# Performance work log

Hardware: AMD Instinct MI355X
Metric: run time of the kernel (lower is better)

## Reference

```python
import jax, jax.numpy as jnp
import numpy as np

N_NODES = 50000


def _gcn_conv(x, src, dst, W, b, n):
    # PyG GCNConv: linear transform, add self-loops, symmetric norm, scatter-sum, bias.
    h = x @ W  # [N, out]
    loop = jnp.arange(n, dtype=src.dtype)
    s = jnp.concatenate([src, loop])
    d = jnp.concatenate([dst, loop])
    deg = jax.ops.segment_sum(jnp.ones_like(d, dtype=h.dtype), d, num_segments=n)
    dinv = jax.lax.rsqrt(jnp.maximum(deg, 1.0))  # deg >= 1 thanks to self-loops
    norm = dinv[s] * dinv[d]  # [E+N]
    msg = h[s] * norm[:, None]
    out = jax.ops.segment_sum(msg, d, num_segments=n)
    return out + b


def setup_inputs() -> dict:
    key = jax.random.key(0)
    ks = jax.random.split(key, 8)
    N, E = N_NODES, 800000
    d_in, d_hid, d_out = 128, 64, 128
    x = jax.random.normal(ks[0], (N, d_in), dtype=jnp.float32)
    edge_index = jax.random.randint(ks[1], (2, E), 0, N, dtype=jnp.int64)
    s = 1.0 / np.sqrt(d_in)
    W1 = jax.random.normal(ks[2], (d_in, d_hid), dtype=jnp.float32) * s
    b1 = jnp.zeros((d_hid,), dtype=jnp.float32)
    Wl = jax.random.normal(ks[3], (d_hid, d_out), dtype=jnp.float32) * (1.0 / np.sqrt(d_hid))
    bl = jnp.zeros((d_out,), dtype=jnp.float32)
    W2 = jax.random.normal(ks[4], (d_hid, d_out), dtype=jnp.float32) * (1.0 / np.sqrt(d_hid))
    b2 = jnp.zeros((d_out,), dtype=jnp.float32)
    return {"x": x, "edge_index": edge_index, "W1": W1, "b1": b1,
            "Wl": Wl, "bl": bl, "W2": W2, "b2": b2}


def reference(x, edge_index, W1, b1, Wl, bl, W2, b2):
    n = x.shape[0]
    src, dst = edge_index[0], edge_index[1]
    h = _gcn_conv(x, src, dst, W1, b1, n)          # conv1 -> [N, 64]
    x1 = h @ Wl + bl                               # residual linear branch [N, 128]
    h = jax.nn.relu(h)
    out = _gcn_conv(h, src, dst, W2, b2, n)        # conv2 -> [N, 128]
    return out + x + x1
```

## Files before the change

kernel.cpp:

```cpp
#include <hip/hip_runtime.h>
#include <hip/hip_fp16.h>

#define DIN 128
#define DH 64
#define DOUT 128
#define STRIDE 64
#define NPART 4


typedef _Float16 f16x8 __attribute__((ext_vector_type(8)));
typedef float f32x4 __attribute__((ext_vector_type(4)));

__global__ __launch_bounds__(256) void k_fill(const int* __restrict__ src,
                                              const int* __restrict__ dst,
                                              int* __restrict__ cnt,
                                              unsigned short* __restrict__ csr,
                                              int E, int n) {
  const int part = blockIdx.x & (NPART - 1);
  const int pb = blockIdx.x >> 2;
  const int nblk = gridDim.x >> 2;
  const int lo = (int)((long)part * n / NPART);
  const int hi = (int)((long)(part + 1) * n / NPART);
  for (int e = pb * 256 + threadIdx.x; e < E; e += nblk * 256) {
    int d = dst[e];
    if (d >= lo && d < hi) {
      int slot = atomicAdd(&cnt[d], 1);
      if (slot < STRIDE) csr[(long)d * STRIDE + slot] = (unsigned short)src[e];
    }
  }
}

__global__ __launch_bounds__(256) void k_gemm1m(const float* __restrict__ x,
                                                const float* __restrict__ W1,
                                                const int* __restrict__ cnt,
                                                __half* __restrict__ h0p, int n) {
  __shared__ _Float16 As[32][DIN + 8];
  __shared__ _Float16 Bt[DH][DIN + 8];
  __shared__ float dds[32];
  const int t = threadIdx.x;
  const int row0 = blockIdx.x * 32;
  if (t < 32) {
    int row = row0 + t;
    dds[t] = (row < n) ? rsqrtf(1.0f + (float)min(cnt[row], STRIDE)) : 0.f;
  }
  for (int i = t; i < DIN * DH; i += 256) {
    int k = i >> 6, c = i & 63;
    Bt[c][k] = (_Float16)W1[i];
  }
  for (int i = t; i < 32 * (DIN / 4); i += 256) {
    int r = i >> 5, k4 = (i & 31) * 4;
    float4 v = make_float4(0.f, 0.f, 0.f, 0.f);
    int row = row0 + r;
    if (row < n) v = *(const float4*)&x[(long)row * DIN + k4];
    As[r][k4 + 0] = (_Float16)v.x; As[r][k4 + 1] = (_Float16)v.y;
    As[r][k4 + 2] = (_Float16)v.z; As[r][k4 + 3] = (_Float16)v.w;
  }
  __syncthreads();

  const int w = t >> 6, l = t & 63;
  const int rg = w & 1;
  const int cg0 = (w >> 1) * 2;
  const int ia = l & 15, kg = l >> 4;
  f32x4 acc0 = {0.f, 0.f, 0.f, 0.f}, acc1 = {0.f, 0.f, 0.f, 0.f};
#pragma unroll
  for (int kb = 0; kb < DIN; kb += 32) {
    f16x8 a  = *(const f16x8*)&As[rg * 16 + ia][kb + kg * 8];
    f16x8 b0 = *(const f16x8*)&Bt[cg0 * 16 + ia][kb + kg * 8];
    f16x8 b1 = *(const f16x8*)&Bt[(cg0 + 1) * 16 + ia][kb + kg * 8];
    acc0 = __builtin_amdgcn_mfma_f32_16x16x32_f16(a, b0, acc0, 0, 0, 0);
    acc1 = __builtin_amdgcn_mfma_f32_16x16x32_f16(a, b1, acc1, 0, 0, 0);
  }
#pragma unroll
  for (int reg = 0; reg < 4; reg++) {
    int rr = rg * 16 + kg * 4 + reg;
    int row = row0 + rr;
    if (row < n) {
      float dd = dds[rr];
      h0p[(long)row * DH + cg0 * 16 + ia] = (__half)(acc0[reg] * dd);
      h0p[(long)row * DH + (cg0 + 1) * 16 + ia] = (__half)(acc1[reg] * dd);
    }
  }
}

__global__ __launch_bounds__(256) void k_gather1(const int* __restrict__ cnt,
                                                 const unsigned short* __restrict__ csr,
                                                 const __half* __restrict__ h0p,
                                                 const float* __restrict__ b1,
                                                 __half* __restrict__ hd, int n) {
  long gid = (long)blockIdx.x * 256 + threadIdx.x;
  int node = (int)(gid >> 3);
  if (node >= n) return;
  int l = (int)(gid & 7);
  const int deg = min(cnt[node], STRIDE);
  const float dd = rsqrtf(1.0f + (float)deg);
  const long base = (long)node * STRIDE;
  float acc[8];
#pragma unroll
  for (int k = 0; k < 8; k++) acc[k] = 0.f;

  auto edge = [&](int s) {
    union { uint4 u; __half2 h[4]; } c;
    c.u = *(const uint4*)&h0p[(long)s * DH + l * 8];
#pragma unroll
    for (int k = 0; k < 4; k++) {
      float2 f = __half22float2(c.h[k]);
      acc[2 * k] += f.x;
      acc[2 * k + 1] += f.y;
    }
  };

  int j = 0;
  for (; j + 4 <= deg; j += 4) {
    ushort4 cs = *(const ushort4*)&csr[base + j];
    edge(cs.x); edge(cs.y); edge(cs.z); edge(cs.w);
  }
  for (; j < deg; j++) edge(csr[base + j]);
  edge(node);

  float4 ba = *(const float4*)&b1[l * 8];
  float4 bb = *(const float4*)&b1[l * 8 + 4];
  float o[8];
  o[0] = acc[0] * dd + ba.x; o[1] = acc[1] * dd + ba.y;
  o[2] = acc[2] * dd + ba.z; o[3] = acc[3] * dd + ba.w;
  o[4] = acc[4] * dd + bb.x; o[5] = acc[5] * dd + bb.y;
  o[6] = acc[6] * dd + bb.z; o[7] = acc[7] * dd + bb.w;
  union { uint4 u; __half2 h[4]; } rv;
#pragma unroll
  for (int k = 0; k < 4; k++)
    rv.h[k] = __floats2half2_rn(o[2 * k] * dd, o[2 * k + 1] * dd);
  *(uint4*)&hd[(long)node * DH + l * 8] = rv.u;
}

__global__ __launch_bounds__(256) void k_gather2C(const int* __restrict__ cnt,
                                                  const unsigned short* __restrict__ csr,
                                                  const __half* __restrict__ hd,
                                                  const float* __restrict__ Wl,
                                                  const float* __restrict__ W2,
                                                  const float* __restrict__ bl,
                                                  const float* __restrict__ b2,
                                                  const float* __restrict__ x,
                                                  float* __restrict__ out, int n) {
  __shared__ float hs[32][DH + 4];
  const int t = threadIdx.x;
  const int row0 = blockIdx.x * 32;

  {
    const int r = t >> 3;
    const int l = t & 7;
    int node = row0 + r;
    float acc[8];
#pragma unroll
    for (int k = 0; k < 8; k++) acc[k] = 0.f;
    float dd = 0.f;
    if (node < n) {
      const int deg = min(cnt[node], STRIDE);
      dd = rsqrtf(1.0f + (float)deg);
      const long base = (long)node * STRIDE;
      auto edge = [&](int s) {
        union { uint4 u; __half2 h[4]; } c;
        c.u = *(const uint4*)&hd[(long)s * DH + l * 8];
#pragma unroll
        for (int k = 0; k < 4; k++) {
          float2 f = __half22float2(c.h[k]);
          acc[2 * k] += fmaxf(f.x, 0.f);
          acc[2 * k + 1] += fmaxf(f.y, 0.f);
        }
      };
      int j = 0;
      for (; j + 4 <= deg; j += 4) {
        ushort4 cs = *(const ushort4*)&csr[base + j];
        edge(cs.x); edge(cs.y); edge(cs.z); edge(cs.w);
      }
      for (; j < deg; j++) edge(csr[base + j]);
      edge(node);
    }
    *(float4*)&hs[r][l * 8] =
        make_float4(acc[0] * dd, acc[1] * dd, acc[2] * dd, acc[3] * dd);
    *(float4*)&hs[r][l * 8 + 4] =
        make_float4(acc[4] * dd, acc[5] * dd, acc[6] * dd, acc[7] * dd);
  }

  const int tc = t & 31, tr = t >> 5;
  const int col4 = tc * 4, r0 = tr * 4;
  float acc[4][4];
#pragma unroll
  for (int r = 0; r < 4; r++)
#pragma unroll
    for (int c = 0; c < 4; c++) acc[r][c] = 0.f;

  __syncthreads();
  for (int k4 = 0; k4 < DH; k4 += 4) {
    float4 hv[4];
#pragma unroll
    for (int r = 0; r < 4; r++) hv[r] = *(const float4*)&hs[r0 + r][k4];
#pragma unroll
    for (int kk = 0; kk < 4; kk++) {
      float4 wv = *(const float4*)&W2[(k4 + kk) * DOUT + col4];
#pragma unroll
      for (int r = 0; r < 4; r++) {
        float hval = (&hv[r].x)[kk];
        acc[r][0] = fmaf(hval, wv.x, acc[r][0]);
        acc[r][1] = fmaf(hval, wv.y, acc[r][1]);
        acc[r][2] = fmaf(hval, wv.z, acc[r][2]);
        acc[r][3] = fmaf(hval, wv.w, acc[r][3]);
      }
    }
  }
  __syncthreads();

  {
    const int r = t >> 3;
    const int l8 = (t & 7) * 8;
    int row = row0 + r;
    float v[8];
#pragma unroll
    for (int k = 0; k < 8; k++) v[k] = 0.f;
    if (row < n) {
      float sc = sqrtf(1.0f + (float)min(cnt[row], STRIDE));
      union { uint4 u; __half2 h[4]; } c;
      c.u = *(const uint4*)&hd[(long)row * DH + l8];
#pragma unroll
      for (int k = 0; k < 4; k++) {
        float2 f = __half22float2(c.h[k]);
        v[2 * k] = f.x * sc;
        v[2 * k + 1] = f.y * sc;
      }
    }
    *(float4*)&hs[r][l8] = make_float4(v[0], v[1], v[2], v[3]);
    *(float4*)&hs[r][l8 + 4] = make_float4(v[4], v[5], v[6], v[7]);
  }
  __syncthreads();
  for (int k4 = 0; k4 < DH; k4 += 4) {
    float4 hv[4];
#pragma unroll
    for (int r = 0; r < 4; r++) hv[r] = *(const float4*)&hs[r0 + r][k4];
#pragma unroll
    for (int kk = 0; kk < 4; kk++) {
      float4 wv = *(const float4*)&Wl[(k4 + kk) * DOUT + col4];
#pragma unroll
      for (int r = 0; r < 4; r++) {
        float hval = (&hv[r].x)[kk];
        acc[r][0] = fmaf(hval, wv.x, acc[r][0]);
        acc[r][1] = fmaf(hval, wv.y, acc[r][1]);
        acc[r][2] = fmaf(hval, wv.z, acc[r][2]);
        acc[r][3] = fmaf(hval, wv.w, acc[r][3]);
      }
    }
  }

  float4 blv = *(const float4*)&bl[col4];
  float4 b2v = *(const float4*)&b2[col4];
#pragma unroll
  for (int r = 0; r < 4; r++) {
    int row = row0 + r0 + r;
    if (row < n) {
      float4 xv = *(const float4*)&x[(long)row * DOUT + col4];
      float4 o;
      o.x = xv.x + acc[r][0] + blv.x + b2v.x;
      o.y = xv.y + acc[r][1] + blv.y + b2v.y;
      o.z = xv.z + acc[r][2] + blv.z + b2v.z;
      o.w = xv.w + acc[r][3] + blv.w + b2v.w;
      *(float4*)&out[(long)row * DOUT + col4] = o;
    }
  }
}

extern "C" void kernel_launch(void* const* d_in, const int* in_sizes, int n_in,
                              void* d_out, int out_size, void* d_ws, size_t ws_size,
                              hipStream_t stream) {
  const float* x = (const float*)d_in[0];
  const int* edge_index = (const int*)d_in[1];
  const float* W1 = (const float*)d_in[2];
  const float* b1 = (const float*)d_in[3];
  const float* Wl = (const float*)d_in[4];
  const float* bl = (const float*)d_in[5];
  const float* W2 = (const float*)d_in[6];
  const float* b2 = (const float*)d_in[7];
  float* out = (float*)d_out;

  const int n = in_sizes[0] / DIN;
  const int E = in_sizes[1] / 2;
  const int* src = edge_index;
  const int* dst = edge_index + E;

  char* p = (char*)d_ws;
  auto alloc = [&](size_t bytes) { char* r = p; p += (bytes + 255) & ~(size_t)255; return r; };
  int* cnt = (int*)alloc((size_t)n * 4);
  unsigned short* csr = (unsigned short*)alloc((size_t)n * STRIDE * 2);
  __half* h0p = (__half*)alloc((size_t)n * DH * 2);
  __half* hd = (__half*)alloc((size_t)n * DH * 2);

  const int B = 256;
  const int blocks32 = (n + 31) / 32;
  hipMemsetAsync(cnt, 0, (size_t)n * sizeof(int), stream);
  k_fill<<<NPART * 256, B, 0, stream>>>(src, dst, cnt, csr, E, n);
  k_gemm1m<<<blocks32, B, 0, stream>>>(x, W1, cnt, h0p, n);
  k_gather1<<<(int)(((long)n * 8 + B - 1) / B), B, 0, stream>>>(cnt, csr, h0p, b1, hd, n);
  k_gather2C<<<blocks32, B, 0, stream>>>(cnt, csr, hd, Wl, W2, bl, b2, x, out, n);
}
```

Measured before the change: 197.0 us.

## Use MFMA f16 matrix cores for fused conv2 and residual GEMMs

Replaces the scalar FP32 FMA loops in the final fused kernel with MFMA 16x16x32 f16 instructions. W2 and Wl are pre-transposed to fp16 by a new small kernel and staged through shared memory. The aggregated features and the rescaled residual input are converted to fp16 as MFMA operands. This removes most of the VALU work in the epilogue GEMMs, at the cost of an extra launch, extra syncs, fp16 rounding of intermediates, and output stores that are no longer vectorised.

After: 188.9 us (median of 2 runs). 1.04x faster.

```diff
diff --git a/kernel.cpp b/kernel.cpp
--- a/kernel.cpp
+++ b/kernel.cpp
@@ -30,6 +30,18 @@
   }
 }
 
+__global__ __launch_bounds__(256) void k_wt(const float* __restrict__ W2,
+                                            const float* __restrict__ Wl,
+                                            __half* __restrict__ Wt2g,
+                                            __half* __restrict__ Wtlg) {
+  int i = blockIdx.x * 256 + threadIdx.x;
+  if (i < DH * DOUT) {
+    int k = i >> 7, c = i & 127;
+    Wt2g[c * DH + k] = __float2half(W2[i]);
+    Wtlg[c * DH + k] = __float2half(Wl[i]);
+  }
+}
+
 __global__ __launch_bounds__(256) void k_gemm1m(const float* __restrict__ x,
                                                 const float* __restrict__ W1,
                                                 const int* __restrict__ cnt,
@@ -131,18 +143,25 @@
   *(uint4*)&hd[(long)node * DH + l * 8] = rv.u;
 }
 
-__global__ __launch_bounds__(256) void k_gather2C(const int* __restrict__ cnt,
+__global__ __launch_bounds__(256) void k_gather2M(const int* __restrict__ cnt,
                                                   const unsigned short* __restrict__ csr,
                                                   const __half* __restrict__ hd,
-                                                  const float* __restrict__ Wl,
-                                                  const float* __restrict__ W2,
+                                                  const __half* __restrict__ Wt2g,
+                                                  const __half* __restrict__ Wtlg,
                                                   const float* __restrict__ bl,
                                                   const float* __restrict__ b2,
                                                   const float* __restrict__ x,
                                                   float* __restrict__ out, int n) {
-  __shared__ float hs[32][DH + 4];
+  __shared__ _Float16 Wt[DOUT][DH + 8];
+  __shared__ _Float16 zs[32][DH + 8];
+  __shared__ float scs[32];
   const int t = threadIdx.x;
   const int row0 = blockIdx.x * 32;
+
+  for (int i = t; i < DOUT * (DH / 8); i += 256) {
+    int c = i >> 3, kq = (i & 7) * 8;
+    *(f16x8*)&Wt[c][kq] = *(const f16x8*)&Wt2g[c * DH + kq];
+  }
 
   {
     const int r = t >> 3;
@@ -174,93 +193,64 @@
       for (; j < deg; j++) edge(csr[base + j]);
       edge(node);
     }
-    *(float4*)&hs[r][l * 8] =
-        make_float4(acc[0] * dd, acc[1] * dd, acc[2] * dd, acc[3] * dd);
-    *(float4*)&hs[r][l * 8 + 4] =
-        make_float4(acc[4] * dd, acc[5] * dd, acc[6] * dd, acc[7] * dd);
-  }
-
-  const int tc = t & 31, tr = t >> 5;
-  const int col4 = tc * 4, r0 = tr * 4;
-  float acc[4][4];
-#pragma unroll
-  for (int r = 0; r < 4; r++)
-#pragma unroll
-    for (int c = 0; c < 4; c++) acc[r][c] = 0.f;
-
-  __syncthreads();
-  for (int k4 = 0; k4 < DH; k4 += 4) {
-    float4 hv[4];
-#pragma unroll
-    for (int r = 0; r < 4; r++) hv[r] = *(const float4*)&hs[r0 + r][k4];
-#pragma unroll
-    for (int kk = 0; kk < 4; kk++) {
-      float4 wv = *(const float4*)&W2[(k4 + kk) * DOUT + col4];
-#pragma unroll
-      for (int r = 0; r < 4; r++) {
-        float hval = (&hv[r].x)[kk];
-        acc[r][0] = fmaf(hval, wv.x, acc[r][0]);
-        acc[r][1] = fmaf(hval, wv.y, acc[r][1]);
-        acc[r][2] = fmaf(hval, wv.z, acc[r][2]);
-        acc[r][3] = fmaf(hval, wv.w, acc[r][3]);
+    if (l == 0)
+      scs[r] = (node < n) ? sqrtf(1.0f + (float)min(cnt[node], STRIDE)) : 0.f;
+    f16x8 zv;
+#pragma unroll
+    for (int k = 0; k < 8; k++) zv[k] = (_Float16)(acc[k] * dd);
+    *(f16x8*)&zs[r][l * 8] = zv;
+  }
+  __syncthreads();
+
+  const int w = t >> 6, l = t & 63;
+  const int rg = w & 1;
+  const int cb = (w >> 1) * 4;
+  const int ia = l & 15, kg = l >> 4;
+  f32x4 acc[4];
+#pragma unroll
+  for (int c = 0; c < 4; c++) acc[c] = (f32x4){0.f, 0.f, 0.f, 0.f};
+
+#pragma unroll
+  for (int kb = 0; kb < DH; kb += 32) {
+    f16x8 a = *(const f16x8*)&zs[rg * 16 + ia][kb + kg * 8];
+#pragma unroll
+    for (int c = 0; c < 4; c++) {
+      f16x8 b = *(const f16x8*)&Wt[(cb + c) * 16 + ia][kb + kg * 8];
+      acc[c] = __builtin_amdgcn_mfma_f32_16x16x32_f16(a, b, acc[c], 0, 0, 0);
+    }
+  }
+  __syncthreads();
+  for (int i = t; i < DOUT * (DH / 8); i += 256) {
+    int c = i >> 3, kq = (i & 7) * 8;
+    *(f16x8*)&Wt[c][kq] = *(const f16x8*)&Wtlg[c * DH + kq];
+  }
+  __syncthreads();
+
+  {
+    int rr = min(row0 + rg * 16 + ia, n - 1);
+    _Float16 sc = (_Float16)scs[rg * 16 + ia];
+    const _Float16* hrow = (const _Float16*)&hd[(long)rr * DH];
+#pragma unroll
+    for (int kb = 0; kb < DH; kb += 32) {
+      f16x8 a = *(const f16x8*)&hrow[kb + kg * 8];
+      a *= sc;
+#pragma unroll
+      for (int c = 0; c < 4; c++) {
+        f16x8 b = *(const f16x8*)&Wt[(cb + c) * 16 + ia][kb + kg * 8];
+        acc[c] = __builtin_amdgcn_mfma_f32_16x16x32_f16(a, b, acc[c], 0, 0, 0);
       }
     }
   }
-  __syncthreads();
-
-  {
-    const int r = t >> 3;
-    const int l8 = (t & 7) * 8;
-    int row = row0 + r;
-    float v[8];
-#pragma unroll
-    for (int k = 0; k < 8; k++) v[k] = 0.f;
-    if (row < n) {
-      float sc = sqrtf(1.0f + (float)min(cnt[row], STRIDE));
-      union { uint4 u; __half2 h[4]; } c;
-      c.u = *(const uint4*)&hd[(long)row * DH + l8];
-#pragma unroll
-      for (int k = 0; k < 4; k++) {
-        float2 f = __half22float2(c.h[k]);
-        v[2 * k] = f.x * sc;
-        v[2 * k + 1] = f.y * sc;
-      }
-    }
-    *(float4*)&hs[r][l8] = make_float4(v[0], v[1], v[2], v[3]);
-    *(float4*)&hs[r][l8 + 4] = make_float4(v[4], v[5], v[6], v[7]);
-  }
-  __syncthreads();
-  for (int k4 = 0; k4 < DH; k4 += 4) {
-    float4 hv[4];
-#pragma unroll
-    for (int r = 0; r < 4; r++) hv[r] = *(const float4*)&hs[r0 + r][k4];
-#pragma unroll
-    for (int kk = 0; kk < 4; kk++) {
-      float4 wv = *(const float4*)&Wl[(k4 + kk) * DOUT + col4];
-#pragma unroll
-      for (int r = 0; r < 4; r++) {
-        float hval = (&hv[r].x)[kk];
-        acc[r][0] = fmaf(hval, wv.x, acc[r][0]);
-        acc[r][1] = fmaf(hval, wv.y, acc[r][1]);
-        acc[r][2] = fmaf(hval, wv.z, acc[r][2]);
-        acc[r][3] = fmaf(hval, wv.w, acc[r][3]);
-      }
-    }
-  }
-
-  float4 blv = *(const float4*)&bl[col4];
-  float4 b2v = *(const float4*)&b2[col4];
-#pragma unroll
-  for (int r = 0; r < 4; r++) {
-    int row = row0 + r0 + r;
-    if (row < n) {
-      float4 xv = *(const float4*)&x[(long)row * DOUT + col4];
-      float4 o;
-      o.x = xv.x + acc[r][0] + blv.x + b2v.x;
-      o.y = xv.y + acc[r][1] + blv.y + b2v.y;
-      o.z = xv.z + acc[r][2] + blv.z + b2v.z;
-      o.w = xv.w + acc[r][3] + blv.w + b2v.w;
-      *(float4*)&out[(long)row * DOUT + col4] = o;
+
+#pragma unroll
+  for (int c = 0; c < 4; c++) {
+    const int col = (cb + c) * 16 + ia;
+    const float bc = bl[col] + b2[col];
+#pragma unroll
+    for (int reg = 0; reg < 4; reg++) {
+      int row = row0 + rg * 16 + kg * 4 + reg;
+      if (row < n)
+        out[(long)row * DOUT + col] = acc[c][reg] + x[(long)row * DOUT + col] + bc;
     }
   }
 }
@@ -289,12 +279,15 @@
   unsigned short* csr = (unsigned short*)alloc((size_t)n * STRIDE * 2);
   __half* h0p = (__half*)alloc((size_t)n * DH * 2);
   __half* hd = (__half*)alloc((size_t)n * DH * 2);
+  __half* Wt2g = (__half*)alloc((size_t)DH * DOUT * 2);
+  __half* Wtlg = (__half*)alloc((size_t)DH * DOUT * 2);
 
   const int B = 256;
   const int blocks32 = (n + 31) / 32;
   hipMemsetAsync(cnt, 0, (size_t)n * sizeof(int), stream);
   k_fill<<<NPART * 256, B, 0, stream>>>(src, dst, cnt, csr, E, n);
+  k_wt<<<(DH * DOUT + B - 1) / B, B, 0, stream>>>(W2, Wl, Wt2g, Wtlg);
   k_gemm1m<<<blocks32, B, 0, stream>>>(x, W1, cnt, h0p, n);
   k_gather1<<<(int)(((long)n * 8 + B - 1) / B), B, 0, stream>>>(cnt, csr, h0p, b1, hd, n);
-  k_gather2C<<<blocks32, B, 0, stream>>>(cnt, csr, hd, Wl, W2, bl, b2, x, out, n);
-}
+  k_gather2M<<<blocks32, B, 0, stream>>>(cnt, csr, hd, Wt2g, Wtlg, bl, b2, x, out, n);
+}
```
